# Kernel tuning notes

Measured on AMD Instinct MI355X. Metric: run time of the kernel, lower is better.

The kernel has to match this reference:

```python
import jax, jax.numpy as jnp
import numpy as np

N_HEAD = 12
D_HEAD = 64
ROT_DIM = 32
THETA = 10000.0
LOOK_B = 1
LOOK_F = 1


def _rope(t):
    # t: [b, h, n, d]; interleaved RoPE on first ROT_DIM dims (lucidrains convention)
    n = t.shape[-2]
    inv_freq = 1.0 / (THETA ** (jnp.arange(0, ROT_DIM, 2, dtype=jnp.float32) / ROT_DIM))
    freqs = jnp.arange(n, dtype=jnp.float32)[:, None] * inv_freq[None, :]   # [n, ROT_DIM//2]
    freqs = jnp.repeat(freqs, 2, axis=-1)                                   # [n, ROT_DIM]
    cos, sin = jnp.cos(freqs), jnp.sin(freqs)
    t_rot, t_pass = t[..., :ROT_DIM], t[..., ROT_DIM:]
    pair = t_rot.reshape(*t_rot.shape[:-1], ROT_DIM // 2, 2)
    rot = jnp.stack([-pair[..., 1], pair[..., 0]], axis=-1).reshape(t_rot.shape)
    return jnp.concatenate([t_rot * cos + rot * sin, t_pass], axis=-1)


def _look_around(x, backward=LOOK_B, forward=LOOK_F, pad_value=-1, dim=2):
    # x: [B, w, n, ...]; pad the window axis, gather shifted windows, concat along dim
    w = x.shape[1]
    pad_width = [(0, 0)] * x.ndim
    pad_width[1] = (backward, forward)
    padded = jnp.pad(x, pad_width, constant_values=pad_value)
    return jnp.concatenate([padded[:, i:i + w] for i in range(forward + backward + 1)], axis=dim)


def _forward(x, w_attn, b_attn, window_size):
    b, n, d_model = x.shape
    qkv = x @ w_attn + b_attn                       # [b, n, 3*d_model]
    q, k, v = jnp.split(qkv, 3, axis=-1)

    def split_heads(t):
        return t.reshape(b, n, N_HEAD, D_HEAD).transpose(0, 2, 1, 3)  # [b, h, n, dh]

    q, k, v = split_heads(q), split_heads(k), split_heads(v)
    q, k = _rope(q), _rope(k)

    scale = D_HEAD ** -0.5
    B = b * N_HEAD
    w = n // window_size
    bq = q.reshape(B, w, window_size, D_HEAD) * scale
    bk = _look_around(k.reshape(B, w, window_size, D_HEAD), pad_value=-1.0)
    bv = _look_around(v.reshape(B, w, window_size, D_HEAD), pad_value=-1.0)

    seq = jnp.arange(n).reshape(1, w, window_size)
    bq_k = _look_around(seq, pad_value=-1)          # [1, w, (lb+lf+1)*ws]
    pad_mask = (bq_k == -1)[:, :, None, :]          # [1, w, 1, j]

    sim = jnp.einsum('bwie,bwje->bwij', bq, bk)     # [B, w, ws, (lb+lf+1)*ws]
    sim = jnp.where(pad_mask, -jnp.finfo(sim.dtype).max, sim)
    attn = jax.nn.softmax(sim, axis=-1)
    out = jnp.einsum('bwij,bwje->bwie', attn, bv)   # [B, w, ws, dh]
    out = out.reshape(b, N_HEAD, n, D_HEAD).transpose(0, 2, 1, 3).reshape(b, n, N_HEAD * D_HEAD)
    return out


def setup_inputs() -> dict:
    key = jax.random.key(0)
    k1, k2, k3 = jax.random.split(key, 3)
    d_model = 768
    x = jax.random.normal(k1, (4, 4096, d_model), dtype=jnp.float32)
    w_attn = jax.random.normal(k2, (d_model, 3 * d_model), dtype=jnp.float32) * 0.02
    b_attn = jax.random.normal(k3, (3 * d_model,), dtype=jnp.float32) * 0.02
    return {"x": x, "w_attn": w_attn, "b_attn": b_attn, "window_size": 128}


def reference(x, w_attn, b_attn, window_size):
    return _forward(x, w_attn, b_attn, window_size)
```

## Files before the change

### kernel.cpp

```cpp
#include <hip/hip_runtime.h>

typedef __attribute__((ext_vector_type(8))) short short8;
typedef __attribute__((ext_vector_type(16))) float f32x16;
typedef __attribute__((ext_vector_type(4))) float f32x4;

__device__ __forceinline__ unsigned short f2bf(float f) {
  unsigned int u = __float_as_uint(f);
  u += 0x7FFFu + ((u >> 16) & 1u);
  return (unsigned short)(u >> 16);
}
__device__ __forceinline__ float bf2f(unsigned short u) {
  return __uint_as_float(((unsigned int)u) << 16);
}

__device__ __forceinline__ void gload16(const unsigned short* g, unsigned short* l) {
  __builtin_amdgcn_global_load_lds(
      (const __attribute__((address_space(1))) void*)g,
      (__attribute__((address_space(3))) void*)l, 16, 0, 0);
}

__global__ __launch_bounds__(256) void cast_x_kernel(const float* __restrict__ x,
                                                     unsigned short* __restrict__ xb,
                                                     int n4) {
  int i = blockIdx.x * 256 + threadIdx.x;
  if (i >= n4) return;
  float4 v = ((const float4*)x)[i];
  ushort4 o;
  o.x = f2bf(v.x); o.y = f2bf(v.y); o.z = f2bf(v.z); o.w = f2bf(v.w);
  ((ushort4*)xb)[i] = o;
}

__global__ void transpose_w_kernel(const float* __restrict__ w,
                                   unsigned short* __restrict__ wt) {
  __shared__ float tile[32][33];
  int n0 = blockIdx.x * 32;
  int k0 = blockIdx.y * 32;
  for (int i = threadIdx.y; i < 32; i += 8)
    tile[i][threadIdx.x] = w[(size_t)(k0 + i) * 2304 + n0 + threadIdx.x];
  __syncthreads();
  for (int i = threadIdx.y; i < 32; i += 8)
    wt[(size_t)(n0 + i) * 768 + k0 + threadIdx.x] = f2bf(tile[threadIdx.x][i]);
}

__global__ __launch_bounds__(256) void qkv_gemm_kernel(
    const unsigned short* __restrict__ xb,
    const unsigned short* __restrict__ wt,
    const float* __restrict__ bias,
    unsigned short* __restrict__ Qb,
    unsigned short* __restrict__ Kb,
    unsigned short* __restrict__ Vb) {
  __shared__ unsigned short lA[128 * 64];
  __shared__ unsigned short lB[128 * 64];
  int bid = blockIdx.x;
  int swz = (bid & 7) * 288 + (bid >> 3);
  int mt = swz / 18, nt = swz - mt * 18;
  int m0 = mt * 128, n0 = nt * 128;

  int tid = threadIdx.x;
  int lane = tid & 63, wid = tid >> 6;
  int wr = wid >> 1, wc = wid & 1;
  int lr = lane & 15, lg = lane >> 4;
  int lswz = lr & 7;

  int offA[4], offB[4];
  unsigned short* ldsA[4];
  unsigned short* ldsB[4];
#pragma unroll
  for (int i = 0; i < 4; i++) {
    int gi = (wid * 4 + i) * 64 + lane;
    int r = gi >> 3;
    int gcl = (gi & 7) ^ (r & 7);
    offA[i] = (m0 + r) * 768 + gcl * 8;
    offB[i] = (n0 + r) * 768 + gcl * 8;
    ldsA[i] = &lA[(wid * 4 + i) * 512];
    ldsB[i] = &lB[(wid * 4 + i) * 512];
  }

  f32x4 acc[4][4] = {};
  const int rowA = (wr * 64 + lr) * 64;
  const int rowB = (wc * 64 + lr) * 64;

  for (int k0 = 0; k0 < 768; k0 += 64) {
    __syncthreads();
#pragma unroll
    for (int i = 0; i < 4; i++) gload16(xb + offA[i] + k0, ldsA[i]);
#pragma unroll
    for (int i = 0; i < 4; i++) gload16(wt + offB[i] + k0, ldsB[i]);
    __syncthreads();

    short8 af[4][2], bfr[4][2];
#pragma unroll
    for (int ks = 0; ks < 2; ks++) {
      int c = ((ks * 4 + lg) ^ lswz) * 8;
#pragma unroll
      for (int mi = 0; mi < 4; mi++)
        af[mi][ks] = *(const short8*)(&lA[rowA + mi * 1024 + c]);
#pragma unroll
      for (int ni = 0; ni < 4; ni++)
        bfr[ni][ks] = *(const short8*)(&lB[rowB + ni * 1024 + c]);
    }
#pragma unroll
    for (int ks = 0; ks < 2; ks++)
#pragma unroll
      for (int mi = 0; mi < 4; mi++)
#pragma unroll
        for (int ni = 0; ni < 4; ni++)
          acc[mi][ni] = __builtin_amdgcn_mfma_f32_16x16x32_bf16(af[mi][ks], bfr[ni][ks], acc[mi][ni], 0, 0, 0);
  }

#pragma unroll
  for (int ni = 0; ni < 4; ni++) {
    int n = n0 + wc * 64 + ni * 16 + lr;
    float bv = bias[n];
    int which = n / 768;
    int idx = n - which * 768;
    int h = idx >> 6, d = idx & 63;
    float scl = (which == 0) ? 0.125f : 1.0f;
    unsigned short* dst = (which == 0) ? Qb : ((which == 1) ? Kb : Vb);
#pragma unroll
    for (int mi = 0; mi < 4; mi++) {
#pragma unroll
      for (int reg = 0; reg < 4; reg++) {
        int m = m0 + wr * 64 + mi * 16 + lg * 4 + reg;
        int b = m >> 12, t = m & 4095;
        dst[(((size_t)(b * 12 + h)) * 4096 + t) * 64 + d] = f2bf((acc[mi][ni][reg] + bv) * scl);
      }
    }
  }
}

__global__ __launch_bounds__(256) void rope_kernel(unsigned short* __restrict__ Qb,
                                                   unsigned short* __restrict__ Kb) {
  const int total = 48 * 4096;
  int r = blockIdx.x * 256 + threadIdx.x;
  if (r >= 2 * total) return;
  bool isQ = (r < total);
  unsigned short* buf = isQ ? Qb : Kb;
  int rr = isQ ? r : (r - total);
  int t = rr & 4095;
  unsigned short* p = buf + (size_t)rr * 64;
  uint4 raw[4];
#pragma unroll
  for (int i = 0; i < 4; i++) raw[i] = ((uint4*)p)[i];
  unsigned short* us = (unsigned short*)raw;
  const float L2T = 13.287712379549449f;
#pragma unroll
  for (int j = 0; j < 16; j++) {
    float inv = exp2f(-(float)j * (L2T / 16.0f));
    float ang = (float)t * inv;
    float s, c;
    sincosf(ang, &s, &c);
    float a = bf2f(us[2 * j]), b = bf2f(us[2 * j + 1]);
    us[2 * j] = f2bf(a * c - b * s);
    us[2 * j + 1] = f2bf(b * c + a * s);
  }
#pragma unroll
  for (int i = 0; i < 4; i++) ((uint4*)p)[i] = raw[i];
}

#define KV_S 72
__global__ __launch_bounds__(256) void attn_kernel(
    const unsigned short* __restrict__ Qb,
    const unsigned short* __restrict__ Kb,
    const unsigned short* __restrict__ Vb,
    float* __restrict__ out) {
  __shared__ unsigned short kS[64 * KV_S];
  __shared__ unsigned short vS[64 * KV_S];
  int wi = blockIdx.x;
  int bh = blockIdx.y;
  int b = bh / 12, h = bh - b * 12;
  int tid = threadIdx.x, lane = tid & 63, wid = tid >> 6;
  int l31 = lane & 31, hi = lane >> 5;

  int qb0 = wi * 128 + wid * 32;
  const unsigned short* Qrow = Qb + ((size_t)bh * 4096 + qb0) * 64;
  short8 qf[4];
#pragma unroll
  for (int kk = 0; kk < 4; kk++)
    qf[kk] = *(const short8*)(Qrow + (size_t)l31 * 64 + kk * 16 + hi * 8);

  f32x16 oacc[2];
#pragma unroll
  for (int dt = 0; dt < 2; dt++)
#pragma unroll
    for (int r = 0; r < 16; r++) oacc[dt][r] = 0.0f;
  float mrow = -1e30f, lsum = 0.0f;

  const unsigned short* Kbase = Kb + (size_t)bh * 4096 * 64;
  const unsigned short* Vbase = Vb + (size_t)bh * 4096 * 64;

  int vk = tid & 63;
  int vq = tid >> 6;

  for (int c = 0; c < 6; c++) {
    int kp0 = (wi - 1) * 128 + c * 64;
    if (kp0 < 0 || kp0 >= 4096) continue;

    __syncthreads();
#pragma unroll
    for (int ci = tid; ci < 512; ci += 256) {
      int kk = ci >> 3, co = (ci & 7) * 8;
      *(uint4*)(&kS[kk * KV_S + co]) = *(const uint4*)(Kbase + (size_t)(kp0 + kk) * 64 + co);
    }
    {
      const unsigned short* vp = Vbase + (size_t)(kp0 + vk) * 64 + vq * 16;
      uint4 v0 = *(const uint4*)(vp);
      uint4 v1 = *(const uint4*)(vp + 8);
      const unsigned short* e = (const unsigned short*)&v0;
#pragma unroll
      for (int i = 0; i < 8; i++) vS[(vq * 16 + i) * KV_S + vk] = e[i];
      e = (const unsigned short*)&v1;
#pragma unroll
      for (int i = 0; i < 8; i++) vS[(vq * 16 + 8 + i) * KV_S + vk] = e[i];
    }
    __syncthreads();

    f32x16 s[2];
#pragma unroll
    for (int kt = 0; kt < 2; kt++) {
      f32x16 acc;
#pragma unroll
      for (int r = 0; r < 16; r++) acc[r] = 0.0f;
#pragma unroll
      for (int kk = 0; kk < 4; kk++) {
        short8 kf = *(const short8*)(&kS[(kt * 32 + l31) * KV_S + kk * 16 + hi * 8]);
        acc = __builtin_amdgcn_mfma_f32_32x32x16_bf16(kf, qf[kk], acc, 0, 0, 0);
      }
      s[kt] = acc;
    }

    float vmax = -1e30f;
#pragma unroll
    for (int kt = 0; kt < 2; kt++)
#pragma unroll
      for (int r = 0; r < 16; r++) vmax = fmaxf(vmax, s[kt][r]);
    vmax = fmaxf(vmax, __shfl_xor(vmax, 32, 64));
    float mnew = fmaxf(mrow, vmax);
    float corr = __expf(mrow - mnew);
    mrow = mnew;
    float rs = 0.0f;
#pragma unroll
    for (int kt = 0; kt < 2; kt++)
#pragma unroll
      for (int r = 0; r < 16; r++) {
        float p = __expf(s[kt][r] - mnew);
        s[kt][r] = p;
        rs += p;
      }
    rs += __shfl_xor(rs, 32, 64);
    lsum = lsum * corr + rs;
#pragma unroll
    for (int dt = 0; dt < 2; dt++)
#pragma unroll
      for (int r = 0; r < 16; r++) oacc[dt][r] *= corr;

#pragma unroll
    for (int kt = 0; kt < 2; kt++) {
#pragma unroll
      for (int kk = 0; kk < 2; kk++) {
        unsigned a0, a1, b0, b1;
        asm("v_cvt_pk_bf16_f32 %0, %1, %2" : "=v"(a0) : "v"(s[kt][kk * 8 + 0]), "v"(s[kt][kk * 8 + 1]));
        asm("v_cvt_pk_bf16_f32 %0, %1, %2" : "=v"(a1) : "v"(s[kt][kk * 8 + 2]), "v"(s[kt][kk * 8 + 3]));
        asm("v_cvt_pk_bf16_f32 %0, %1, %2" : "=v"(b0) : "v"(s[kt][kk * 8 + 4]), "v"(s[kt][kk * 8 + 5]));
        asm("v_cvt_pk_bf16_f32 %0, %1, %2" : "=v"(b1) : "v"(s[kt][kk * 8 + 6]), "v"(s[kt][kk * 8 + 7]));
        asm("v_permlane32_swap_b32 %0, %1" : "+v"(a0), "+v"(b0));
        asm("v_permlane32_swap_b32 %0, %1" : "+v"(a1), "+v"(b1));
        union { unsigned u[4]; short8 v; } pb;
        pb.u[0] = a0; pb.u[1] = a1; pb.u[2] = b0; pb.u[3] = b1;
#pragma unroll
        for (int dt = 0; dt < 2; dt++) {
          short8 vf = *(const short8*)(&vS[(dt * 32 + l31) * KV_S + kt * 32 + kk * 16 + hi * 8]);
          oacc[dt] = __builtin_amdgcn_mfma_f32_32x32x16_bf16(vf, pb.v, oacc[dt], 0, 0, 0);
        }
      }
    }
  }

  float inv = 1.0f / lsum;
  float* orow = out + ((size_t)b * 4096 + qb0 + l31) * 768 + h * 64;
#pragma unroll
  for (int dt = 0; dt < 2; dt++)
#pragma unroll
    for (int g = 0; g < 4; g++) {
      float4 o;
      o.x = oacc[dt][g * 4 + 0] * inv;
      o.y = oacc[dt][g * 4 + 1] * inv;
      o.z = oacc[dt][g * 4 + 2] * inv;
      o.w = oacc[dt][g * 4 + 3] * inv;
      *(float4*)(orow + dt * 32 + g * 8 + hi * 4) = o;
    }
}

extern "C" void kernel_launch(void* const* d_in, const int* in_sizes, int n_in,
                              void* d_out, int out_size, void* d_ws, size_t ws_size,
                              hipStream_t stream) {
  const float* x = (const float*)d_in[0];
  const float* w = (const float*)d_in[1];
  const float* bias = (const float*)d_in[2];
  float* out = (float*)d_out;

  char* ws = (char*)d_ws;
  unsigned short* xb = (unsigned short*)ws;
  unsigned short* wt = (unsigned short*)(ws + 25165824);
  unsigned short* Qb = (unsigned short*)(ws + 25165824 + 3538944);
  unsigned short* Kb = Qb + 12582912;
  unsigned short* Vb = Kb + 12582912;

  hipLaunchKernelGGL(cast_x_kernel, dim3(12288), dim3(256), 0, stream, x, xb, 3145728);
  hipLaunchKernelGGL(transpose_w_kernel, dim3(72, 24), dim3(32, 8), 0, stream, w, wt);
  hipLaunchKernelGGL(qkv_gemm_kernel, dim3(2304), dim3(256), 0, stream, xb, wt, bias, Qb, Kb, Vb);
  hipLaunchKernelGGL(rope_kernel, dim3(1536), dim3(256), 0, stream, Qb, Kb);
  hipLaunchKernelGGL(attn_kernel, dim3(32, 48), dim3(256), 0, stream, Qb, Kb, Vb, out);
}
```

Before: 152.5 us.

## Fuse RoPE into QKV GEMM epilogue using precomputed cos/sin table

Removes the standalone RoPE kernel and applies the rotation inside the QKV GEMM epilogue. Adjacent-pair values are exchanged with a lane shuffle, and cos/sin come from a small precomputed table built by a new kernel. This avoids a full extra read and write of Q and K in bf16 and the per-element sincos work. In exchange it adds shuffles and table loads to the GEMM epilogue plus one tiny extra launch.

```diff
diff --git a/kernel.cpp b/kernel.cpp
--- a/kernel.cpp
+++ b/kernel.cpp
@@ -17,6 +17,17 @@
   __builtin_amdgcn_global_load_lds(
       (const __attribute__((address_space(1))) void*)g,
       (__attribute__((address_space(3))) void*)l, 16, 0, 0);
+}
+
+__global__ __launch_bounds__(256) void rope_table_kernel(float2* __restrict__ tbl) {
+  int i = blockIdx.x * 256 + threadIdx.x;
+  int t = i >> 4, j = i & 15;
+  const float L2T = 13.287712379549449f;
+  float inv = exp2f(-(float)j * (L2T / 16.0f));
+  float ang = (float)t * inv;
+  float s, c;
+  sincosf(ang, &s, &c);
+  tbl[i] = make_float2(c, s);
 }
 
 __global__ __launch_bounds__(256) void cast_x_kernel(const float* __restrict__ x,
@@ -46,6 +57,7 @@
     const unsigned short* __restrict__ xb,
     const unsigned short* __restrict__ wt,
     const float* __restrict__ bias,
+    const float2* __restrict__ tbl,
     unsigned short* __restrict__ Qb,
     unsigned short* __restrict__ Kb,
     unsigned short* __restrict__ Vb) {
@@ -116,6 +128,9 @@
     int idx = n - which * 768;
     int h = idx >> 6, d = idx & 63;
     float scl = (which == 0) ? 0.125f : 1.0f;
+    bool doRope = (which < 2) && (ni < 2);
+    int jj = d >> 1;
+    bool isHi = (d & 1);
     unsigned short* dst = (which == 0) ? Qb : ((which == 1) ? Kb : Vb);
 #pragma unroll
     for (int mi = 0; mi < 4; mi++) {
@@ -123,39 +138,16 @@
       for (int reg = 0; reg < 4; reg++) {
         int m = m0 + wr * 64 + mi * 16 + lg * 4 + reg;
         int b = m >> 12, t = m & 4095;
-        dst[(((size_t)(b * 12 + h)) * 4096 + t) * 64 + d] = f2bf((acc[mi][ni][reg] + bv) * scl);
+        float val = acc[mi][ni][reg] + bv;
+        if (doRope) {
+          float other = __shfl_xor(val, 1, 64);
+          float2 cs = tbl[(t << 4) + jj];
+          val = isHi ? (val * cs.x + other * cs.y) : (val * cs.x - other * cs.y);
+        }
+        dst[(((size_t)(b * 12 + h)) * 4096 + t) * 64 + d] = f2bf(val * scl);
       }
     }
   }
-}
-
-__global__ __launch_bounds__(256) void rope_kernel(unsigned short* __restrict__ Qb,
-                                                   unsigned short* __restrict__ Kb) {
-  const int total = 48 * 4096;
-  int r = blockIdx.x * 256 + threadIdx.x;
-  if (r >= 2 * total) return;
-  bool isQ = (r < total);
-  unsigned short* buf = isQ ? Qb : Kb;
-  int rr = isQ ? r : (r - total);
-  int t = rr & 4095;
-  unsigned short* p = buf + (size_t)rr * 64;
-  uint4 raw[4];
-#pragma unroll
-  for (int i = 0; i < 4; i++) raw[i] = ((uint4*)p)[i];
-  unsigned short* us = (unsigned short*)raw;
-  const float L2T = 13.287712379549449f;
-#pragma unroll
-  for (int j = 0; j < 16; j++) {
-    float inv = exp2f(-(float)j * (L2T / 16.0f));
-    float ang = (float)t * inv;
-    float s, c;
-    sincosf(ang, &s, &c);
-    float a = bf2f(us[2 * j]), b = bf2f(us[2 * j + 1]);
-    us[2 * j] = f2bf(a * c - b * s);
-    us[2 * j + 1] = f2bf(b * c + a * s);
-  }
-#pragma unroll
-  for (int i = 0; i < 4; i++) ((uint4*)p)[i] = raw[i];
 }
 
 #define KV_S 72
@@ -302,13 +294,14 @@
   char* ws = (char*)d_ws;
   unsigned short* xb = (unsigned short*)ws;
   unsigned short* wt = (unsigned short*)(ws + 25165824);
-  unsigned short* Qb = (unsigned short*)(ws + 25165824 + 3538944);
+  unsigned short* Qb = (unsigned short*)(ws + 28704768);
   unsigned short* Kb = Qb + 12582912;
   unsigned short* Vb = Kb + 12582912;
-
+  float2* tbl = (float2*)(ws + 104202240);
+
+  hipLaunchKernelGGL(rope_table_kernel, dim3(256), dim3(256), 0, stream, tbl);
   hipLaunchKernelGGL(cast_x_kernel, dim3(12288), dim3(256), 0, stream, x, xb, 3145728);
   hipLaunchKernelGGL(transpose_w_kernel, dim3(72, 24), dim3(32, 8), 0, stream, w, wt);
-  hipLaunchKernelGGL(qkv_gemm_kernel, dim3(2304), dim3(256), 0, stream, xb, wt, bias, Qb, Kb, Vb);
-  hipLaunchKernelGGL(rope_kernel, dim3(1536), dim3(256), 0, stream, Qb, Kb);
+  hipLaunchKernelGGL(qkv_gemm_kernel, dim3(2304), dim3(256), 0, stream, xb, wt, bias, tbl, Qb, Kb, Vb);
   hipLaunchKernelGGL(attn_kernel, dim3(32, 48), dim3(256), 0, stream, Qb, Kb, Vb, out);
 }
```

Result: slower. 170.1 us (+11.5%).
